# Kernel tuning notes

Measured on AMD Instinct MI355X. Metric: run time of the kernel, lower is better.

The kernel has to match this reference:

```python
import jax, jax.numpy as jnp
import numpy as np

EPS_NORM = 1e-5

def conv1x1(x, W, b):
    # 1x1 conv == per-pixel linear: [b,c,h,w] x [o,c] -> [b,o,h,w]
    return jnp.einsum('bchw,oc->bohw', x, W) + b[None, :, None, None]

def mean_variance_norm(feat, eps=1e-5):
    # torch .var(dim=2) is unbiased (ddof=1)
    b, c = feat.shape[:2]
    flat = feat.reshape(b, c, -1)
    mean = flat.mean(axis=2)
    std = jnp.sqrt(flat.var(axis=2, ddof=1) + eps)
    return (feat - mean[:, :, None, None]) / std[:, :, None, None]


def setup_inputs() -> dict:
    key = jax.random.key(0)
    ks = jax.random.split(key, 10)
    B, Cin, Ck, H, W = 4, 512, 512, 64, 64
    sc = 1.0 / np.sqrt(Ck)
    return {
        'content':     jax.random.normal(ks[0], (B, Cin, H, W), jnp.float32),
        'style':       jax.random.normal(ks[1], (B, Cin, H, W), jnp.float32),
        'content_key': jax.random.normal(ks[2], (B, Ck, H, W), jnp.float32),
        'style_key':   jax.random.normal(ks[3], (B, Ck, H, W), jnp.float32),
        'Wf': jax.random.normal(ks[4], (Ck, Ck), jnp.float32) * sc,
        'bf': jax.random.normal(ks[5], (Ck,), jnp.float32) * 0.01,
        'Wg': jax.random.normal(ks[6], (Ck, Ck), jnp.float32) * sc,
        'bg': jax.random.normal(ks[7], (Ck,), jnp.float32) * 0.01,
        'Wh': jax.random.normal(ks[8], (Cin, Cin), jnp.float32) * sc,
        'bh': jax.random.normal(ks[9], (Cin,), jnp.float32) * 0.01,
    }


def reference(content, style, content_key, style_key, Wf, bf, Wg, bg, Wh, bh):
    F = conv1x1(content_key, Wf, bf)   # [b,Ck,h,w]
    G = conv1x1(style_key, Wg, bg)     # [b,Ck,hg,wg]
    Hs = conv1x1(style, Wh, bh)        # [b,Cin,hg,wg]
    b, Ck, h, w = F.shape
    hg, wg = G.shape[2], G.shape[3]
    M = hg * wg
    Gf = G.reshape(b, Ck, M)                              # [b,Ck,M]
    style_flat = Hs.reshape(b, -1, M).transpose(0, 2, 1)  # [b,M,Cin]
    G_norm = jnp.sqrt((Gf ** 2).sum(axis=1))[:, None, :]  # [b,1,M]
    Ff = F.reshape(b, Ck, h * w)
    F_norm = jnp.sqrt((Ff ** 2).sum(axis=1))[:, :, None]  # [b,N,1]
    Ft = Ff.transpose(0, 2, 1)                            # [b,N,Ck]
    # cosine-similarity affinity, shifted + relu instead of softmax
    S = jax.nn.relu(jnp.matmul(Ft, Gf) / (F_norm + EPS_NORM) / (G_norm + EPS_NORM) + 1.0)
    S = S / (S.sum(axis=-1, keepdims=True) + EPS_NORM)    # [b,N,M]
    mean = jnp.matmul(S, style_flat)                      # [b,N,Cin]
    std = jnp.sqrt(jax.nn.relu(jnp.matmul(S, style_flat ** 2) - mean ** 2))
    mean = mean.reshape(b, h, w, -1).transpose(0, 3, 1, 2)
    std = std.reshape(b, h, w, -1).transpose(0, 3, 1, 2)
    return std * mean_variance_norm(content) + mean
```

## Files before the change

### kernel.cpp

```cpp
#include <hip/hip_runtime.h>
#include <hip/hip_bf16.h>
#include <math.h>

#define B_SZ 4
#define CDIM 512
#define NPIX 4096
#define EPSN 1e-5f

typedef unsigned short u16;
typedef __attribute__((ext_vector_type(8))) short bf16x8;
typedef __attribute__((ext_vector_type(4))) float f32x4;
typedef __attribute__((ext_vector_type(16))) float f32x16;

#define MFMA_BF16 __builtin_amdgcn_mfma_f32_16x16x32_bf16
#define MFMA32    __builtin_amdgcn_mfma_f32_32x32x16_bf16

#define GLD16(gp, lp) __builtin_amdgcn_global_load_lds( \
    (const __attribute__((address_space(1))) void*)(gp), \
    (__attribute__((address_space(3))) void*)(lp), 16, 0, 0)

static __device__ __forceinline__ float bf2f(u16 u) {
    return __uint_as_float(((unsigned)u) << 16);
}
static __device__ __forceinline__ u16 f2bf(float f) {
    unsigned u = __float_as_uint(f);
    unsigned r = (u + 0x7FFFu + ((u >> 16) & 1u)) >> 16;
    return (u16)r;
}
static __device__ __forceinline__ bf16x8 sq_bf16x8(bf16x8 a) {
    union { bf16x8 v; unsigned w[4]; } in, out;
    in.v = a;
    #pragma unroll
    for (int k = 0; k < 4; k++) {
        unsigned wl = in.w[k] << 16;
        unsigned wh = in.w[k] & 0xFFFF0000u;
        float sl = __uint_as_float(wl); sl *= sl;
        float sh = __uint_as_float(wh); sh *= sh;
        out.w[k] = (__float_as_uint(sh) & 0xFFFF0000u) | (__float_as_uint(sl) >> 16);
    }
    return out.v;
}

__global__ __launch_bounds__(256) void transpose3b(const float* __restrict__ X0,
    const float* __restrict__ X1, const float* __restrict__ X2,
    u16* __restrict__ XTbase, int bg0)
{
    const int z = blockIdx.z;
    const int gb = z / 3, which = z % 3;
    const size_t TBe = (size_t)CDIM * NPIX;
    const float* X = (which == 0 ? X0 : which == 1 ? X1 : X2) + (size_t)(bg0 + gb) * TBe;
    u16* XT = XTbase + (size_t)z * TBe;

    __shared__ float T[64][65];
    const int t = threadIdx.x;
    const int n0 = blockIdx.x * 64, c0 = blockIdx.y * 64;
    #pragma unroll
    for (int p = 0; p < 4; p++) {
        int c_l = (t >> 4) + p * 16;
        int n_l = (t & 15) * 4;
        float4 v = *(const float4*)&X[(size_t)(c0 + c_l) * NPIX + n0 + n_l];
        T[c_l][n_l+0] = v.x; T[c_l][n_l+1] = v.y; T[c_l][n_l+2] = v.z; T[c_l][n_l+3] = v.w;
    }
    __syncthreads();
    #pragma unroll
    for (int p = 0; p < 4; p++) {
        int n_l = t >> 2;
        int cs  = (t & 3) * 4 + p * 16;
        ushort4 r;
        r.x = f2bf(T[cs+0][n_l]); r.y = f2bf(T[cs+1][n_l]);
        r.z = f2bf(T[cs+2][n_l]); r.w = f2bf(T[cs+3][n_l]);
        *(ushort4*)&XT[(size_t)(n0 + n_l) * CDIM + c0 + cs] = r;
    }
}

__global__ __launch_bounds__(256) void conv3b(const u16* __restrict__ XTbase,
    const float* __restrict__ W0, const float* __restrict__ W1, const float* __restrict__ W2,
    const float* __restrict__ b0, const float* __restrict__ b1, const float* __restrict__ b2,
    u16* __restrict__ FTb, u16* __restrict__ GTb, u16* __restrict__ Hbb)
{
    const int z = blockIdx.z;
    const int gb = z / 3, which = z % 3;
    const size_t TBe = (size_t)CDIM * NPIX;
    const u16* XT = XTbase + (size_t)z * TBe;
    const float* W = which == 0 ? W0 : which == 1 ? W1 : W2;
    const float* bias = which == 0 ? b0 : which == 1 ? b1 : b2;

    const int t = threadIdx.x;
    const int lane = t & 63, wv = t >> 6;
    const int wr = wv >> 1, wc = wv & 1;
    const int n0 = blockIdx.x * 64;
    const int o0 = blockIdx.y * 64;
    const int g = lane >> 4, li = lane & 15;

    __shared__ short Aw[64][40];
    __shared__ short Bx[64][40];

    f32x4 acc[2][2] = {};
    const int srow = t >> 2, sseg = (t & 3) * 8;

    float4 w0 = *(const float4*)&W[(size_t)(o0 + srow) * CDIM + sseg];
    float4 w1 = *(const float4*)&W[(size_t)(o0 + srow) * CDIM + sseg + 4];
    bf16x8 bv = *(const bf16x8*)&XT[(size_t)(n0 + srow) * CDIM + sseg];

    for (int kb = 0; kb < CDIM; kb += 32) {
        bf16x8 wa;
        wa[0] = (short)f2bf(w0.x); wa[1] = (short)f2bf(w0.y);
        wa[2] = (short)f2bf(w0.z); wa[3] = (short)f2bf(w0.w);
        wa[4] = (short)f2bf(w1.x); wa[5] = (short)f2bf(w1.y);
        wa[6] = (short)f2bf(w1.z); wa[7] = (short)f2bf(w1.w);
        __syncthreads();
        *(bf16x8*)&Aw[srow][sseg] = wa;
        *(bf16x8*)&Bx[srow][sseg] = bv;
        if (kb + 32 < CDIM) {
            w0 = *(const float4*)&W[(size_t)(o0 + srow) * CDIM + kb + 32 + sseg];
            w1 = *(const float4*)&W[(size_t)(o0 + srow) * CDIM + kb + 32 + sseg + 4];
            bv = *(const bf16x8*)&XT[(size_t)(n0 + srow) * CDIM + kb + 32 + sseg];
        }
        __syncthreads();
        bf16x8 a[2], b[2];
        #pragma unroll
        for (int i = 0; i < 2; i++) a[i] = *(const bf16x8*)&Aw[wr*32 + i*16 + li][g*8];
        #pragma unroll
        for (int j = 0; j < 2; j++) b[j] = *(const bf16x8*)&Bx[wc*32 + j*16 + li][g*8];
        #pragma unroll
        for (int i = 0; i < 2; i++)
            #pragma unroll
            for (int j = 0; j < 2; j++)
                acc[i][j] = MFMA_BF16(a[i], b[j], acc[i][j], 0, 0, 0);
    }

    #pragma unroll
    for (int i = 0; i < 2; i++) {
        const int orow = o0 + wr*32 + i*16 + 4*g;
        float4 bs = *(const float4*)&bias[orow];
        #pragma unroll
        for (int j = 0; j < 2; j++) {
            const int ncol = n0 + wc*32 + j*16 + li;
            if (which < 2) {
                u16* Y = (which == 0 ? FTb : GTb) + (size_t)gb * TBe;
                ushort4 r;
                r.x = f2bf(acc[i][j][0] + bs.x);
                r.y = f2bf(acc[i][j][1] + bs.y);
                r.z = f2bf(acc[i][j][2] + bs.z);
                r.w = f2bf(acc[i][j][3] + bs.w);
                *(ushort4*)&Y[(size_t)ncol * CDIM + orow] = r;
            } else {
                u16* Y2 = Hbb + (size_t)gb * TBe;
                const float bb[4] = { bs.x, bs.y, bs.z, bs.w };
                #pragma unroll
                for (int r = 0; r < 4; r++)
                    Y2[(size_t)(orow + r) * NPIX + ncol] = f2bf(acc[i][j][r] + bb[r]);
            }
        }
    }
}

__global__ __launch_bounds__(256) void norm2b(const u16* __restrict__ FT,
    const u16* __restrict__ GT, float* __restrict__ Fn, float* __restrict__ Gn,
    float* __restrict__ rs)
{
    const int gb = blockIdx.y >> 1, z = blockIdx.y & 1;
    const size_t TBe = (size_t)CDIM * NPIX;
    const int n = blockIdx.x * 256 + threadIdx.x;
    const u16* row = ((z ? GT : FT) + (size_t)gb * TBe) + (size_t)n * CDIM;
    float s = 0.f;
    for (int c = 0; c < CDIM; c += 8) {
        bf16x8 v = *(const bf16x8*)&row[c];
        #pragma unroll
        for (int e = 0; e < 8; e++) { float f = bf2f((u16)v[e]); s += f * f; }
    }
    ((z ? Gn : Fn) + (size_t)gb * NPIX)[n] = sqrtf(s);
    if (!z) rs[(size_t)gb * NPIX + n] = 0.f;
}

__global__ __launch_bounds__(256) void s_gemm128(const u16* __restrict__ FTb,
    const u16* __restrict__ GTb, const float* __restrict__ Fnb, const float* __restrict__ Gnb,
    u16* __restrict__ Sbase, float* __restrict__ rsb, int strip_base, int swz,
    size_t s_stride)
{
    const int gb = blockIdx.y;
    const size_t TBe = (size_t)CDIM * NPIX;
    const u16* FT = FTb + (size_t)gb * TBe;
    const u16* GT = GTb + (size_t)gb * TBe;
    const float* Fn = Fnb + (size_t)gb * NPIX;
    const float* Gn = Gnb + (size_t)gb * NPIX;
    u16* S = Sbase + (size_t)gb * s_stride;
    float* rs = rsb + (size_t)gb * NPIX;

    const int t = threadIdx.x;
    const int lane = t & 63, wv = t >> 6;
    const int wr = wv >> 1, wc = wv & 1;

    int mm, nn;
    if (swz) {
        const int xk = blockIdx.x & 7, q = blockIdx.x >> 3;
        mm = q & 31;
        nn = (q >> 5) * 8 + xk;
    } else {
        mm = blockIdx.x & 31;
        nn = blockIdx.x >> 5;
    }
    const int m0  = mm * 128;
    const int nl0 = nn * 128;
    const int ng0 = strip_base + nl0;
    const int g = lane >> 4, li = lane & 15;

    __shared__ short Cs[2][128][64];

    f32x4 acc[4][4] = {};

    const int lr = lane >> 3, lq = lane & 7;

    #define SG_STAGE(BUF, KB)                                                  \
    {                                                                          \
        _Pragma("unroll")                                                      \
        for (int ch = 0; ch < 4; ch++) {                                       \
            const int r0 = wv*32 + ch*8;                                       \
            const int r  = r0 + lr;                                            \
            const int c  = lq ^ (r & 7);                                       \
            const u16* gp = (c < 4)                                            \
                ? &FT[(size_t)(ng0 + r) * CDIM + (KB) + c*8]                   \
                : &GT[(size_t)(m0  + r) * CDIM + (KB) + (c-4)*8];              \
            GLD16(gp, &Cs[BUF][r0][0]);                                        \
        }                                                                      \
    }

    SG_STAGE(0, 0);
    __syncthreads();

    int buf = 0;
    for (int kb = 0; kb < CDIM; kb += 32) {
        if (kb + 32 < CDIM) SG_STAGE(buf ^ 1, kb + 32);
        bf16x8 a[4], b[4];
        #pragma unroll
        for (int i = 0; i < 4; i++) {
            const int row = wr*64 + i*16 + li;
            a[i] = *(const bf16x8*)&Cs[buf][row][(g ^ (row & 7)) * 8];
        }
        #pragma unroll
        for (int j = 0; j < 4; j++) {
            const int row = wc*64 + j*16 + li;
            b[j] = *(const bf16x8*)&Cs[buf][row][((4 + g) ^ (row & 7)) * 8];
        }
        #pragma unroll
        for (int i = 0; i < 4; i++)
            #pragma unroll
            for (int j = 0; j < 4; j++)
                acc[i][j] = MFMA_BF16(a[i], b[j], acc[i][j], 0, 0, 0);
        __syncthreads();
        buf ^= 1;
    }
    #undef SG_STAGE

    float gi[4];
    #pragma unroll
    for (int j = 0; j < 4; j++) gi[j] = 1.f / (Gn[m0 + wc*64 + j*16 + li] + EPSN);
    #pragma unroll
    for (int i = 0; i < 4; i++) {
        const int nl = nl0 + wr*64 + i*16 + 4*g;
        float4 fn4 = *(const float4*)&Fn[strip_base + nl];
        const float fi4[4] = { 1.f/(fn4.x + EPSN), 1.f/(fn4.y + EPSN),
                               1.f/(fn4.z + EPSN), 1.f/(fn4.w + EPSN) };
        float ps[4] = {0.f, 0.f, 0.f, 0.f};
        #pragma unroll
        for (int j = 0; j < 4; j++) {
            const int m = m0 + wc*64 + j*16 + li;
            #pragma unroll
            for (int r = 0; r < 4; r++) {
                float v = fmaxf(acc[i][j][r] * fi4[r] * gi[j] + 1.f, 0.f);
                u16 hv = f2bf(v);
                S[(size_t)(nl + r) * NPIX + m] = hv;
                ps[r] += bf2f(hv);
            }
        }
        #pragma unroll
        for (int r = 0; r < 4; r++) {
            float p = ps[r];
            p += __shfl_xor(p, 1);
            p += __shfl_xor(p, 2);
            p += __shfl_xor(p, 4);
            p += __shfl_xor(p, 8);
            if (li == 0) atomicAdd(&rs[strip_base + nl + r], p);
        }
    }
}

__global__ __launch_bounds__(256) void pv64(const u16* __restrict__ Hbb,
    const u16* __restrict__ Sbase, const float* __restrict__ rsb,
    const float* __restrict__ content, const float* __restrict__ mub,
    const float* __restrict__ isdb, float* __restrict__ out, int strip_base,
    int bg0, size_t s_stride)
{
    const int gb = blockIdx.y;
    const size_t TBe = (size_t)CDIM * NPIX;
    const u16* Hb = Hbb + (size_t)gb * TBe;
    const u16* Sb = Sbase + (size_t)gb * s_stride;
    const float* rs = rsb + (size_t)gb * NPIX;
    const float* content_b = content + (size_t)(bg0 + gb) * TBe;
    const float* mu  = mub  + (size_t)(bg0 + gb) * CDIM;
    const float* isd = isdb + (size_t)(bg0 + gb) * CDIM;
    float* out_b = out + (size_t)(bg0 + gb) * TBe;

    const int t = threadIdx.x;
    const int lane = t & 63, wv = t >> 6;
    const int wr = wv >> 1, wc = wv & 1;
    const int l31 = lane & 31, h = lane >> 5;

    const int xk = blockIdx.x & 7, q = blockIdx.x >> 3;
    const int c0  = (q & 7) * 64;
    const int nl0 = ((q >> 3) * 8 + xk) * 64;

    __shared__ short AS[2][64][128];

    f32x16 am = {}, aq = {};

    const int lr = lane >> 4, lq = lane & 15;

    #define PV_STAGE(BUF, KB)                                                  \
    {                                                                          \
        _Pragma("unroll")                                                      \
        for (int ch = 0; ch < 4; ch++) {                                       \
            const int r0 = wv*16 + ch*4;                                       \
            const int r  = r0 + lr;                                            \
            const int c  = lq ^ (r & 15);                                      \
            const u16* gp = (c < 8)                                            \
                ? &Hb[(size_t)(c0  + r) * NPIX + (KB) + c*8]                   \
                : &Sb[(size_t)(nl0 + r) * NPIX + (KB) + (c-8)*8];              \
            GLD16(gp, &AS[BUF][r0][0]);                                        \
        }                                                                      \
    }

    const int ra = wr*32 + l31, rb = wc*32 + l31;
    const int swa = (ra & 15) << 4, swb = (rb & 15) << 4;

    PV_STAGE(0, 0);
    __syncthreads();

    int buf = 0;
    for (int kb = 0; kb < NPIX; kb += 64) {
        if (kb + 64 < NPIX) PV_STAGE(buf ^ 1, kb + 64);
        const short* rpa = &AS[buf][ra][0];
        const short* rpb = &AS[buf][rb][0];
        #pragma unroll
        for (int ks = 0; ks < 4; ks++) {
            bf16x8 a  = *(const bf16x8*)&rpa[((ks*32 + h*16      ) ^ swa) >> 1];
            bf16x8 b  = *(const bf16x8*)&rpb[((ks*32 + h*16 + 128) ^ swb) >> 1];
            bf16x8 a2 = sq_bf16x8(a);
            am = MFMA32(a,  b, am, 0, 0, 0);
            aq = MFMA32(a2, b, aq, 0, 0, 0);
        }
        __syncthreads();
        buf ^= 1;
    }
    #undef PV_STAGE

    const int n = strip_base + nl0 + wc*32 + l31;
    const float inv = 1.f / (rs[n] + EPSN);
    #pragma unroll
    for (int qd = 0; qd < 4; qd++) {
        const int cb = c0 + wr*32 + 8*qd + 4*h;
        float4 mu4 = *(const float4*)&mu[cb];
        float4 is4 = *(const float4*)&isd[cb];
        const float muA[4] = { mu4.x, mu4.y, mu4.z, mu4.w };
        const float isA[4] = { is4.x, is4.y, is4.z, is4.w };
        #pragma unroll
        for (int r2 = 0; r2 < 4; r2++) {
            const int reg = qd*4 + r2;
            float mean = am[reg] * inv;
            float msq  = aq[reg] * inv;
            float sd   = sqrtf(fmaxf(msq - mean*mean, 0.f));
            float cv   = content_b[(size_t)(cb + r2) * NPIX + n];
            out_b[(size_t)(cb + r2) * NPIX + n] = sd * (cv - muA[r2]) * isA[r2] + mean;
        }
    }
}

__global__ __launch_bounds__(256) void content_stats(const float* __restrict__ x,
    float* __restrict__ mu, float* __restrict__ isd)
{
    const int bc = blockIdx.x;
    const int tid = threadIdx.x;
    const float* row = x + (size_t)bc * NPIX;
    float s = 0.f, s2 = 0.f;
    for (int i = tid * 4; i < NPIX; i += 256 * 4) {
        float4 v = *(const float4*)&row[i];
        s  += v.x + v.y + v.z + v.w;
        s2 += v.x*v.x + v.y*v.y + v.z*v.z + v.w*v.w;
    }
    __shared__ float r1[256], r2[256];
    r1[tid] = s; r2[tid] = s2; __syncthreads();
    for (int st = 128; st; st >>= 1) {
        if (tid < st) { r1[tid] += r1[tid+st]; r2[tid] += r2[tid+st]; }
        __syncthreads();
    }
    if (tid == 0) {
        float m = r1[0] / NPIX;
        float var = (r2[0] - (float)NPIX * m * m) / (float)(NPIX - 1);
        mu[bc]  = m;
        isd[bc] = rsqrtf(var + 1e-5f);
    }
}

extern "C" void kernel_launch(void* const* d_in, const int* in_sizes, int n_in,
                              void* d_out, int out_size, void* d_ws, size_t ws_size,
                              hipStream_t stream)
{
    const float* content     = (const float*)d_in[0];
    const float* style       = (const float*)d_in[1];
    const float* content_key = (const float*)d_in[2];
    const float* style_key   = (const float*)d_in[3];
    const float* Wf  = (const float*)d_in[4];
    const float* bf_ = (const float*)d_in[5];
    const float* Wg  = (const float*)d_in[6];
    const float* bg  = (const float*)d_in[7];
    const float* Wh  = (const float*)d_in[8];
    const float* bh  = (const float*)d_in[9];
    float* out = (float*)d_out;

    const size_t TB = (size_t)CDIM * NPIX;
    const size_t tail_bytes = (3 * (size_t)B_SZ * NPIX + 2 * (size_t)B_SZ * CDIM) * 4 + 256;

    int nb = 1, ns = 512;
    {
        const int nbc[5] = {4, 2, 4, 2, 1};
        const int nsc[5] = {4096, 4096, 2048, 2048, 4096};
        bool found = false;
        for (int i = 0; i < 5; i++) {
            size_t need = (size_t)nbc[i] * (6 * TB + (size_t)NPIX * nsc[i]) * 2 + tail_bytes;
            if (need <= ws_size) { nb = nbc[i]; ns = nsc[i]; found = true; break; }
        }
        if (!found) {
            nb = 1;
            for (int cand = 2048; cand >= 512; cand >>= 1) {
                size_t need = (6 * TB + (size_t)NPIX * cand) * 2 + tail_bytes;
                if (need <= ws_size) { ns = cand; break; }
            }
        }
    }
    const size_t s_stride = (size_t)NPIX * ns;

    u16* FT  = (u16*)d_ws;
    u16* GT  = FT + (size_t)nb * TB;
    u16* Hb  = GT + (size_t)nb * TB;
    u16* XT  = Hb + (size_t)nb * TB;
    u16* Sb  = XT + (size_t)nb * 3 * TB;
    float* Fn  = (float*)(Sb + (size_t)nb * s_stride);
    float* Gn  = Fn + (size_t)B_SZ * NPIX;
    float* rsb = Gn + (size_t)B_SZ * NPIX;
    float* mu  = rsb + (size_t)B_SZ * NPIX;
    float* isd = mu + (size_t)B_SZ * CDIM;

    content_stats<<<B_SZ * CDIM, 256, 0, stream>>>(content, mu, isd);

    const int sg_swz = ((ns / 128) % 8 == 0) ? 1 : 0;
    const int sg_blocks = (NPIX / 128) * (ns / 128);
    const int pv_blocks = 8 * (ns / 64);

    for (int bg0 = 0; bg0 < B_SZ; bg0 += nb) {
        const int g = (bg0 + nb <= B_SZ) ? nb : (B_SZ - bg0);

        transpose3b<<<dim3(NPIX/64, CDIM/64, 3*g), 256, 0, stream>>>(
                content_key, style_key, style, XT, bg0);

        conv3b<<<dim3(NPIX/64, CDIM/64, 3*g), 256, 0, stream>>>(
                XT, Wf, Wg, Wh, bf_, bg, bh, FT, GT, Hb);

        norm2b<<<dim3(NPIX/256, 2*g), 256, 0, stream>>>(FT, GT, Fn, Gn, rsb);

        for (int s0 = 0; s0 < NPIX; s0 += ns) {
            s_gemm128<<<dim3(sg_blocks, g), 256, 0, stream>>>(FT, GT, Fn, Gn,
                    Sb, rsb, s0, sg_swz, s_stride);
            pv64<<<dim3(pv_blocks, g), 256, 0, stream>>>(Hb, Sb, rsb,
                    content, mu, isd, out, s0, bg0, s_stride);
        }
    }
}
```

Measured before the change: 428.0 us.

## Widen PV kernel tile to 64x128 to reuse H and squared-H operands

The PV GEMM kernel now computes a 64-channel by 128-pixel tile per block instead of 64x64. Each wave loads one H fragment and its square, then reuses them across two S fragments, so squaring work and H traffic per output are halved. The LDS tile grows to 96 rows, launch bounds request 3 blocks per CU, and block swizzling becomes conditional. The bf16 squaring pack also switches to a single byte-permute instruction. In exchange, register pressure rises and there are half as many blocks, which may reduce occupancy and load balance.

After: 411.0 us. -4.0%, faster.

```diff
diff --git a/kernel.cpp b/kernel.cpp
--- a/kernel.cpp
+++ b/kernel.cpp
@@ -36,7 +36,8 @@
         unsigned wh = in.w[k] & 0xFFFF0000u;
         float sl = __uint_as_float(wl); sl *= sl;
         float sh = __uint_as_float(wh); sh *= sh;
-        out.w[k] = (__float_as_uint(sh) & 0xFFFF0000u) | (__float_as_uint(sl) >> 16);
+        out.w[k] = __builtin_amdgcn_perm(__float_as_uint(sh), __float_as_uint(sl),
+                                         0x07060302u);
     }
     return out.v;
 }
@@ -285,11 +286,11 @@
     }
 }
 
-__global__ __launch_bounds__(256) void pv64(const u16* __restrict__ Hbb,
+__global__ __launch_bounds__(256, 3) void pv64x128(const u16* __restrict__ Hbb,
     const u16* __restrict__ Sbase, const float* __restrict__ rsb,
     const float* __restrict__ content, const float* __restrict__ mub,
     const float* __restrict__ isdb, float* __restrict__ out, int strip_base,
-    int bg0, size_t s_stride)
+    int bg0, size_t s_stride, int swz)
 {
     const int gb = blockIdx.y;
     const size_t TBe = (size_t)CDIM * NPIX;
@@ -306,32 +307,51 @@
     const int wr = wv >> 1, wc = wv & 1;
     const int l31 = lane & 31, h = lane >> 5;
 
-    const int xk = blockIdx.x & 7, q = blockIdx.x >> 3;
-    const int c0  = (q & 7) * 64;
-    const int nl0 = ((q >> 3) * 8 + xk) * 64;
-
-    __shared__ short AS[2][64][128];
-
-    f32x16 am = {}, aq = {};
+    int c_t, n_t;
+    if (swz) {
+        const int xk = blockIdx.x & 7, q = blockIdx.x >> 3;
+        c_t = q & 7;
+        n_t = (q >> 3) * 8 + xk;
+    } else {
+        c_t = blockIdx.x & 7;
+        n_t = blockIdx.x >> 3;
+    }
+    const int c0  = c_t * 64;
+    const int nl0 = n_t * 128;
+
+    __shared__ short AS[2][96][128];
+
+    f32x16 am0 = {}, am1 = {}, aq0 = {}, aq1 = {};
 
     const int lr = lane >> 4, lq = lane & 15;
 
     #define PV_STAGE(BUF, KB)                                                  \
     {                                                                          \
         _Pragma("unroll")                                                      \
-        for (int ch = 0; ch < 4; ch++) {                                       \
-            const int r0 = wv*16 + ch*4;                                       \
+        for (int ch = 0; ch < 6; ch++) {                                       \
+            const int r0 = wv*24 + ch*4;                                       \
             const int r  = r0 + lr;                                            \
             const int c  = lq ^ (r & 15);                                      \
-            const u16* gp = (c < 8)                                            \
-                ? &Hb[(size_t)(c0  + r) * NPIX + (KB) + c*8]                   \
-                : &Sb[(size_t)(nl0 + r) * NPIX + (KB) + (c-8)*8];              \
+            const u16* gp;                                                     \
+            if (r0 < 64)                                                       \
+                gp = (c < 8)                                                   \
+                    ? &Hb[(size_t)(c0  + r) * NPIX + (KB) + c*8]               \
+                    : &Sb[(size_t)(nl0 + r) * NPIX + (KB) + (c-8)*8];          \
+            else                                                               \
+                gp = (c < 8)                                                   \
+                    ? &Sb[(size_t)(nl0 + r     ) * NPIX + (KB) + c*8]          \
+                    : &Sb[(size_t)(nl0 + r + 32) * NPIX + (KB) + (c-8)*8];     \
             GLD16(gp, &AS[BUF][r0][0]);                                        \
         }                                                                      \
     }
 
-    const int ra = wr*32 + l31, rb = wc*32 + l31;
-    const int swa = (ra & 15) << 4, swb = (rb & 15) << 4;
+    const int prow_a  = wr*32 + l31;
+    const int prow_b0 = wc ? (64 + l31) : l31;
+    const int sb_b0   = wc ? 0 : 8;
+    const int prow_b1 = wc ? (64 + l31) : (32 + l31);
+    const int swa  = prow_a  & 15;
+    const int swb0 = prow_b0 & 15;
+    const int swb1 = prow_b1 & 15;
 
     PV_STAGE(0, 0);
     __syncthreads();
@@ -339,38 +359,48 @@
     int buf = 0;
     for (int kb = 0; kb < NPIX; kb += 64) {
         if (kb + 64 < NPIX) PV_STAGE(buf ^ 1, kb + 64);
-        const short* rpa = &AS[buf][ra][0];
-        const short* rpb = &AS[buf][rb][0];
+        const short* rpa  = &AS[buf][prow_a ][0];
+        const short* rpb0 = &AS[buf][prow_b0][0];
+        const short* rpb1 = &AS[buf][prow_b1][0];
         #pragma unroll
         for (int ks = 0; ks < 4; ks++) {
-            bf16x8 a  = *(const bf16x8*)&rpa[((ks*32 + h*16      ) ^ swa) >> 1];
-            bf16x8 b  = *(const bf16x8*)&rpb[((ks*32 + h*16 + 128) ^ swb) >> 1];
+            const int sg = ks*2 + h;
+            bf16x8 a  = *(const bf16x8*)&rpa [((sg        ) ^ swa ) * 8];
+            bf16x8 b0 = *(const bf16x8*)&rpb0[((sb_b0 + sg) ^ swb0) * 8];
+            bf16x8 b1 = *(const bf16x8*)&rpb1[((8     + sg) ^ swb1) * 8];
             bf16x8 a2 = sq_bf16x8(a);
-            am = MFMA32(a,  b, am, 0, 0, 0);
-            aq = MFMA32(a2, b, aq, 0, 0, 0);
+            am0 = MFMA32(a,  b0, am0, 0, 0, 0);
+            am1 = MFMA32(a,  b1, am1, 0, 0, 0);
+            aq0 = MFMA32(a2, b0, aq0, 0, 0, 0);
+            aq1 = MFMA32(a2, b1, aq1, 0, 0, 0);
         }
         __syncthreads();
         buf ^= 1;
     }
     #undef PV_STAGE
 
-    const int n = strip_base + nl0 + wc*32 + l31;
-    const float inv = 1.f / (rs[n] + EPSN);
-    #pragma unroll
-    for (int qd = 0; qd < 4; qd++) {
-        const int cb = c0 + wr*32 + 8*qd + 4*h;
-        float4 mu4 = *(const float4*)&mu[cb];
-        float4 is4 = *(const float4*)&isd[cb];
-        const float muA[4] = { mu4.x, mu4.y, mu4.z, mu4.w };
-        const float isA[4] = { is4.x, is4.y, is4.z, is4.w };
-        #pragma unroll
-        for (int r2 = 0; r2 < 4; r2++) {
-            const int reg = qd*4 + r2;
-            float mean = am[reg] * inv;
-            float msq  = aq[reg] * inv;
-            float sd   = sqrtf(fmaxf(msq - mean*mean, 0.f));
-            float cv   = content_b[(size_t)(cb + r2) * NPIX + n];
-            out_b[(size_t)(cb + r2) * NPIX + n] = sd * (cv - muA[r2]) * isA[r2] + mean;
+    #pragma unroll
+    for (int j = 0; j < 2; j++) {
+        const int n = strip_base + nl0 + wc*64 + j*32 + l31;
+        const float inv = 1.f / (rs[n] + EPSN);
+        const f32x16& am = j ? am1 : am0;
+        const f32x16& aq = j ? aq1 : aq0;
+        #pragma unroll
+        for (int qd = 0; qd < 4; qd++) {
+            const int cb = c0 + wr*32 + 8*qd + 4*h;
+            float4 mu4 = *(const float4*)&mu[cb];
+            float4 is4 = *(const float4*)&isd[cb];
+            const float muA[4] = { mu4.x, mu4.y, mu4.z, mu4.w };
+            const float isA[4] = { is4.x, is4.y, is4.z, is4.w };
+            #pragma unroll
+            for (int r2 = 0; r2 < 4; r2++) {
+                const int reg = qd*4 + r2;
+                float mean = am[reg] * inv;
+                float msq  = aq[reg] * inv;
+                float sd   = sqrtf(fmaxf(msq - mean*mean, 0.f));
+                float cv   = content_b[(size_t)(cb + r2) * NPIX + n];
+                out_b[(size_t)(cb + r2) * NPIX + n] = sd * (cv - muA[r2]) * isA[r2] + mean;
+            }
         }
     }
 }
@@ -454,7 +484,8 @@
 
     const int sg_swz = ((ns / 128) % 8 == 0) ? 1 : 0;
     const int sg_blocks = (NPIX / 128) * (ns / 128);
-    const int pv_blocks = 8 * (ns / 64);
+    const int pv_swz = ((ns / 128) % 8 == 0) ? 1 : 0;
+    const int pv_blocks = 8 * (ns / 128);
 
     for (int bg0 = 0; bg0 < B_SZ; bg0 += nb) {
         const int g = (bg0 + nb <= B_SZ) ? nb : (B_SZ - bg0);
@@ -470,8 +501,8 @@
         for (int s0 = 0; s0 < NPIX; s0 += ns) {
             s_gemm128<<<dim3(sg_blocks, g), 256, 0, stream>>>(FT, GT, Fn, Gn,
                     Sb, rsb, s0, sg_swz, s_stride);
-            pv64<<<dim3(pv_blocks, g), 256, 0, stream>>>(Hb, Sb, rsb,
-                    content, mu, isd, out, s0, bg0, s_stride);
-        }
-    }
-}
+            pv64x128<<<dim3(pv_blocks, g), 256, 0, stream>>>(Hb, Sb, rsb,
+                    content, mu, isd, out, s0, bg0, s_stride, pv_swz);
+        }
+    }
+}
```

## Enlarge PV GEMM tile to 128x128 with 2x2 MFMA blocking per wave

Applied to the files above, without the earlier changes.

The P·V kernel now computes 128x128 output tiles instead of 64x64. Each wave holds a 2x2 set of 32x32 MFMA accumulators for both mean and second moment, which raises operand reuse from LDS and halves the global reloads of S and H. A block-index swizzle is added for cache locality, and the bf16 squaring pack now uses a single perm instruction. The cost is more registers and twice the LDS per block, which may lower occupancy, and fewer blocks, which may underfill the GPU for small strips.

New measurement: 387.5 us. -9.5%, faster.

```diff
diff --git a/kernel.cpp b/kernel.cpp
--- a/kernel.cpp
+++ b/kernel.cpp
@@ -36,7 +36,8 @@
         unsigned wh = in.w[k] & 0xFFFF0000u;
         float sl = __uint_as_float(wl); sl *= sl;
         float sh = __uint_as_float(wh); sh *= sh;
-        out.w[k] = (__float_as_uint(sh) & 0xFFFF0000u) | (__float_as_uint(sl) >> 16);
+        out.w[k] = __builtin_amdgcn_perm(__float_as_uint(sh), __float_as_uint(sl),
+                                         0x07060302u);
     }
     return out.v;
 }
@@ -285,11 +286,11 @@
     }
 }
 
-__global__ __launch_bounds__(256) void pv64(const u16* __restrict__ Hbb,
+__global__ __launch_bounds__(256, 2) void pv128(const u16* __restrict__ Hbb,
     const u16* __restrict__ Sbase, const float* __restrict__ rsb,
     const float* __restrict__ content, const float* __restrict__ mub,
     const float* __restrict__ isdb, float* __restrict__ out, int strip_base,
-    int bg0, size_t s_stride)
+    int bg0, size_t s_stride, int swz)
 {
     const int gb = blockIdx.y;
     const size_t TBe = (size_t)CDIM * NPIX;
@@ -306,21 +307,31 @@
     const int wr = wv >> 1, wc = wv & 1;
     const int l31 = lane & 31, h = lane >> 5;
 
-    const int xk = blockIdx.x & 7, q = blockIdx.x >> 3;
-    const int c0  = (q & 7) * 64;
-    const int nl0 = ((q >> 3) * 8 + xk) * 64;
-
-    __shared__ short AS[2][64][128];
-
-    f32x16 am = {}, aq = {};
+    int c_t, n_t;
+    if (swz) {
+        const int chunk = (int)gridDim.x >> 3;
+        const int id = (blockIdx.x & 7) * chunk + (blockIdx.x >> 3);
+        c_t = id & 3;
+        n_t = id >> 2;
+    } else {
+        c_t = blockIdx.x & 3;
+        n_t = blockIdx.x >> 2;
+    }
+    const int c0  = c_t * 128;
+    const int nl0 = n_t * 128;
+
+    __shared__ short AS[2][128][128];
+
+    f32x16 am[2][2] = {};
+    f32x16 aq[2][2] = {};
 
     const int lr = lane >> 4, lq = lane & 15;
 
     #define PV_STAGE(BUF, KB)                                                  \
     {                                                                          \
         _Pragma("unroll")                                                      \
-        for (int ch = 0; ch < 4; ch++) {                                       \
-            const int r0 = wv*16 + ch*4;                                       \
+        for (int ch = 0; ch < 8; ch++) {                                       \
+            const int r0 = wv*32 + ch*4;                                       \
             const int r  = r0 + lr;                                            \
             const int c  = lq ^ (r & 15);                                      \
             const u16* gp = (c < 8)                                            \
@@ -330,47 +341,63 @@
         }                                                                      \
     }
 
-    const int ra = wr*32 + l31, rb = wc*32 + l31;
-    const int swa = (ra & 15) << 4, swb = (rb & 15) << 4;
-
     PV_STAGE(0, 0);
     __syncthreads();
 
     int buf = 0;
     for (int kb = 0; kb < NPIX; kb += 64) {
         if (kb + 64 < NPIX) PV_STAGE(buf ^ 1, kb + 64);
-        const short* rpa = &AS[buf][ra][0];
-        const short* rpb = &AS[buf][rb][0];
         #pragma unroll
         for (int ks = 0; ks < 4; ks++) {
-            bf16x8 a  = *(const bf16x8*)&rpa[((ks*32 + h*16      ) ^ swa) >> 1];
-            bf16x8 b  = *(const bf16x8*)&rpb[((ks*32 + h*16 + 128) ^ swb) >> 1];
-            bf16x8 a2 = sq_bf16x8(a);
-            am = MFMA32(a,  b, am, 0, 0, 0);
-            aq = MFMA32(a2, b, aq, 0, 0, 0);
+            const int sg = ks*2 + h;
+            bf16x8 a[2], a2[2], b[2];
+            #pragma unroll
+            for (int i = 0; i < 2; i++) {
+                const int q = wr*64 + i*32 + l31;
+                a[i]  = *(const bf16x8*)&AS[buf][q][(sg ^ (q & 15)) * 8];
+                a2[i] = sq_bf16x8(a[i]);
+            }
+            #pragma unroll
+            for (int j = 0; j < 2; j++) {
+                const int q = wc*64 + j*32 + l31;
+                b[j] = *(const bf16x8*)&AS[buf][q][((8 + sg) ^ (q & 15)) * 8];
+            }
+            #pragma unroll
+            for (int i = 0; i < 2; i++)
+                #pragma unroll
+                for (int j = 0; j < 2; j++) {
+                    am[i][j] = MFMA32(a[i],  b[j], am[i][j], 0, 0, 0);
+                    aq[i][j] = MFMA32(a2[i], b[j], aq[i][j], 0, 0, 0);
+                }
         }
         __syncthreads();
         buf ^= 1;
     }
     #undef PV_STAGE
 
-    const int n = strip_base + nl0 + wc*32 + l31;
-    const float inv = 1.f / (rs[n] + EPSN);
-    #pragma unroll
-    for (int qd = 0; qd < 4; qd++) {
-        const int cb = c0 + wr*32 + 8*qd + 4*h;
-        float4 mu4 = *(const float4*)&mu[cb];
-        float4 is4 = *(const float4*)&isd[cb];
-        const float muA[4] = { mu4.x, mu4.y, mu4.z, mu4.w };
-        const float isA[4] = { is4.x, is4.y, is4.z, is4.w };
-        #pragma unroll
-        for (int r2 = 0; r2 < 4; r2++) {
-            const int reg = qd*4 + r2;
-            float mean = am[reg] * inv;
-            float msq  = aq[reg] * inv;
-            float sd   = sqrtf(fmaxf(msq - mean*mean, 0.f));
-            float cv   = content_b[(size_t)(cb + r2) * NPIX + n];
-            out_b[(size_t)(cb + r2) * NPIX + n] = sd * (cv - muA[r2]) * isA[r2] + mean;
+    #pragma unroll
+    for (int j = 0; j < 2; j++) {
+        const int n = strip_base + nl0 + wc*64 + j*32 + l31;
+        const float inv = 1.f / (rs[n] + EPSN);
+        #pragma unroll
+        for (int i = 0; i < 2; i++) {
+            #pragma unroll
+            for (int qd = 0; qd < 4; qd++) {
+                const int cb = c0 + wr*64 + i*32 + 8*qd + 4*h;
+                float4 mu4 = *(const float4*)&mu[cb];
+                float4 is4 = *(const float4*)&isd[cb];
+                const float muA[4] = { mu4.x, mu4.y, mu4.z, mu4.w };
+                const float isA[4] = { is4.x, is4.y, is4.z, is4.w };
+                #pragma unroll
+                for (int r2 = 0; r2 < 4; r2++) {
+                    const int reg = qd*4 + r2;
+                    float mean = am[i][j][reg] * inv;
+                    float msq  = aq[i][j][reg] * inv;
+                    float sd   = sqrtf(fmaxf(msq - mean*mean, 0.f));
+                    float cv   = content_b[(size_t)(cb + r2) * NPIX + n];
+                    out_b[(size_t)(cb + r2) * NPIX + n] = sd * (cv - muA[r2]) * isA[r2] + mean;
+                }
+            }
         }
     }
 }
@@ -454,7 +481,8 @@
 
     const int sg_swz = ((ns / 128) % 8 == 0) ? 1 : 0;
     const int sg_blocks = (NPIX / 128) * (ns / 128);
-    const int pv_blocks = 8 * (ns / 64);
+    const int pv_blocks = (CDIM / 128) * (ns / 128);
+    const int pv_swz = (pv_blocks % 8 == 0) ? 1 : 0;
 
     for (int bg0 = 0; bg0 < B_SZ; bg0 += nb) {
         const int g = (bg0 + nb <= B_SZ) ? nb : (B_SZ - bg0);
@@ -470,8 +498,8 @@
         for (int s0 = 0; s0 < NPIX; s0 += ns) {
             s_gemm128<<<dim3(sg_blocks, g), 256, 0, stream>>>(FT, GT, Fn, Gn,
                     Sb, rsb, s0, sg_swz, s_stride);
-            pv64<<<dim3(pv_blocks, g), 256, 0, stream>>>(Hb, Sb, rsb,
-                    content, mu, isd, out, s0, bg0, s_stride);
-        }
-    }
-}
+            pv128<<<dim3(pv_blocks, g), 256, 0, stream>>>(Hb, Sb, rsb,
+                    content, mu, isd, out, s0, bg0, s_stride, pv_swz);
+        }
+    }
+}
```
